# Kernel optimization log

Measured on AMD Instinct MI355X. Metric: run time of the kernel, lower is better.

Reference implementation:

```python
import jax, jax.numpy as jnp
import numpy as np

D_MODEL = 256
NHEAD = 4
K_MODE = 8


def setup_inputs() -> dict:
    key = jax.random.key(0)
    ks = jax.random.split(key, 12)
    bs, S = 2, 4096
    inp = {
        "q": jax.random.normal(ks[0], (bs, S, D_MODEL), jnp.float32),
        "k": jax.random.normal(ks[1], (bs, S, D_MODEL + K_MODE), jnp.float32),
        "v": jax.random.normal(ks[2], (bs, S, D_MODEL), jnp.float32),
        "mask": jax.random.randint(ks[3], (bs, S, S), 0, 2, jnp.int32),
        # nn.Linear params: W is [out, in], y = x @ W.T + b
        "Wq": jax.random.normal(ks[4], (D_MODEL, D_MODEL), jnp.float32) * 0.02,
        "bq": jnp.zeros((D_MODEL,), jnp.float32),
        "Wk": jax.random.normal(ks[5], (D_MODEL, D_MODEL + K_MODE), jnp.float32) * 0.02,
        "bk": jnp.zeros((D_MODEL,), jnp.float32),
        "Wv": jax.random.normal(ks[6], (D_MODEL, D_MODEL), jnp.float32) * 0.02,
        "bv": jnp.zeros((D_MODEL,), jnp.float32),
        "Wo": jax.random.normal(ks[7], (D_MODEL, NHEAD * D_MODEL), jnp.float32) * 0.02,
        "bo": jnp.zeros((D_MODEL,), jnp.float32),
    }
    return inp


def reference(q, k, v, mask, Wq, bq, Wk, bk, Wv, bv, Wo, bo):
    # Projections (nn.Linear: x @ W.T + b). In the original module the projected
    # q/k/v are repeat-broadcast identically across all nhead heads (d_k = d_model),
    # and the mask broadcasts across heads too (dropout disabled). Hence every head
    # computes the exact same attention output; we compute it once and tile the
    # concat, which is mathematically identical and avoids redundant HBM traffic.
    qh = jnp.einsum('bsd,ed->bse', q, Wq) + bq   # [bs, S, d]
    kh = jnp.einsum('bsd,ed->bse', k, Wk) + bk   # [bs, S, d]
    vh = jnp.einsum('bsd,ed->bse', v, Wv) + bv   # [bs, S, d]

    scale = 1.0 / jnp.sqrt(jnp.asarray(D_MODEL, qh.dtype))
    scores = jnp.einsum('bqd,bkd->bqk', qh, kh) * scale  # [bs, S, S]
    scores = jnp.where(mask == 0, jnp.asarray(-1e9, scores.dtype), scores)
    attn = jax.nn.softmax(scores, axis=-1)
    per_head = jnp.einsum('bqk,bkd->bqd', attn, vh)      # [bs, S, d]

    concat = jnp.tile(per_head, (1, 1, NHEAD))           # [bs, S, h*d]
    return jnp.einsum('bsf,df->bsd', concat, Wo) + bo
```

## Files before the change

### kernel.cpp

```cpp
#include <hip/hip_runtime.h>

typedef unsigned short u16;
typedef unsigned int u32;
typedef unsigned long long u64;
typedef __bf16 bf16x8 __attribute__((ext_vector_type(8)));
typedef float f32x4 __attribute__((ext_vector_type(4)));

#define S_LEN 4096
#define DM 256

__device__ __forceinline__ u16 f2b(float f) {
  u32 u = __builtin_bit_cast(u32, f);
  u = (u + 0x7FFFu + ((u >> 16) & 1u)) >> 16;
  return (u16)u;
}
__device__ __forceinline__ float b2f(u16 b) {
  return __builtin_bit_cast(float, (u32)b << 16);
}

__device__ __forceinline__ f32x4 mfma16(bf16x8 a, bf16x8 b, f32x4 c) {
  return __builtin_amdgcn_mfma_f32_16x16x32_bf16(a, b, c, 0, 0, 0);
}

__device__ __forceinline__ void gl_lds16(const u16* g, u16* l) {
  __builtin_amdgcn_global_load_lds(
      (const __attribute__((address_space(1))) u32*)g,
      (__attribute__((address_space(3))) u32*)l, 16, 0, 0);
}

#define SB() __builtin_amdgcn_sched_barrier(0)

template <int TIN_F32, int TOUT_F32, int BIAS_MODE>
__global__ __launch_bounds__(256, 2) void gemm_nt_kernel(
    const void* __restrict__ Ap, const void* __restrict__ Bp,
    void* __restrict__ Cp, const float* __restrict__ bias, float scale,
    int M, int N, int K, int lda, int ldb, int ldc,
    long sA, long sB, long sC) {
  __shared__ u16 As[64][72];
  __shared__ u16 Bs[64][72];
  const int tid = threadIdx.x;
  const int w = tid >> 6, ln = tid & 63, lg = ln >> 4, ll = ln & 15;
  const int m0 = blockIdx.x * 64, n0 = blockIdx.y * 64;
  const long zA = (long)blockIdx.z * sA, zB = (long)blockIdx.z * sB,
             zC = (long)blockIdx.z * sC;

  const f32x4 fzero = {0.f, 0.f, 0.f, 0.f};
  f32x4 acc[4];
#pragma unroll
  for (int i = 0; i < 4; ++i) acc[i] = fzero;

  const int srow = tid >> 2, scb = (tid & 3) * 16;
  const int nk = (K + 63) >> 6;
  for (int kc = 0; kc < nk; ++kc) {
    const int k0 = kc * 64;
    if (TIN_F32) {
      {
        const float* src = (const float*)Ap + zA + (size_t)(m0 + srow) * lda + k0 + scb;
        u16 t[16];
        if (k0 + 64 <= K) {
#pragma unroll
          for (int i = 0; i < 16; ++i) t[i] = f2b(src[i]);
        } else {
#pragma unroll
          for (int i = 0; i < 16; ++i) {
            int gk = k0 + scb + i;
            t[i] = (gk < K) ? f2b(src[i]) : (u16)0;
          }
        }
#pragma unroll
        for (int i = 0; i < 16; ++i) As[srow][scb + i] = t[i];
      }
      {
        const float* src = (const float*)Bp + zB + (size_t)(n0 + srow) * ldb + k0 + scb;
        u16 t[16];
        if (k0 + 64 <= K) {
#pragma unroll
          for (int i = 0; i < 16; ++i) t[i] = f2b(src[i]);
        } else {
#pragma unroll
          for (int i = 0; i < 16; ++i) {
            int gk = k0 + scb + i;
            t[i] = (gk < K) ? f2b(src[i]) : (u16)0;
          }
        }
#pragma unroll
        for (int i = 0; i < 16; ++i) Bs[srow][scb + i] = t[i];
      }
    } else {
      const u16* srcA = (const u16*)Ap + zA + (size_t)(m0 + srow) * lda + k0 + scb;
      *(bf16x8*)&As[srow][scb] = *(const bf16x8*)srcA;
      *(bf16x8*)&As[srow][scb + 8] = *(const bf16x8*)(srcA + 8);
      const u16* srcB = (const u16*)Bp + zB + (size_t)(n0 + srow) * ldb + k0 + scb;
      *(bf16x8*)&Bs[srow][scb] = *(const bf16x8*)srcB;
      *(bf16x8*)&Bs[srow][scb + 8] = *(const bf16x8*)(srcB + 8);
    }
    __syncthreads();
#pragma unroll
    for (int ks = 0; ks < 2; ++ks) {
      bf16x8 af = *(const bf16x8*)&As[w * 16 + ll][ks * 32 + lg * 8];
#pragma unroll
      for (int ct = 0; ct < 4; ++ct) {
        bf16x8 bfr = *(const bf16x8*)&Bs[ct * 16 + ll][ks * 32 + lg * 8];
        acc[ct] = mfma16(af, bfr, acc[ct]);
      }
    }
    __syncthreads();
  }

#pragma unroll
  for (int ct = 0; ct < 4; ++ct) {
#pragma unroll
    for (int j = 0; j < 4; ++j) {
      int row = m0 + w * 16 + lg * 4 + j;
      int col = n0 + ct * 16 + ll;
      float v = acc[ct][j];
      if (BIAS_MODE == 1) v += bias[col];
      if (BIAS_MODE == 2) v += bias[row];
      v *= scale;
      if (TOUT_F32)
        ((float*)Cp)[zC + (size_t)row * ldc + col] = v;
      else
        ((u16*)Cp)[zC + (size_t)row * ldc + col] = f2b(v);
    }
  }
}

__global__ void wos_kernel(const float* __restrict__ Wo, u16* __restrict__ WoS) {
  int d = blockIdx.x, e = threadIdx.x;
  const float* p = Wo + (size_t)d * 1024;
  WoS[(size_t)d * 256 + e] = f2b(p[e] + p[256 + e] + p[512 + e] + p[768 + e]);
}

__global__ __launch_bounds__(256) void bitpack_kernel(const int* __restrict__ mask,
                                                      u32* __restrict__ mb) {
  const int ln = threadIdx.x & 63;
  const int gw = (int)((blockIdx.x * 256 + threadIdx.x) >> 6);
  const int nw = gridDim.x * 4;
  u64* mb64 = (u64*)mb;
  for (int it = gw; it < 131072; it += nw) {
    const int* p = mask + (size_t)it * 256 + ln;
    int v0 = p[0], v1 = p[64], v2 = p[128], v3 = p[192];
    u64 b0 = __ballot(v0 != 0);
    u64 b1 = __ballot(v1 != 0);
    u64 b2 = __ballot(v2 != 0);
    u64 b3 = __ballot(v3 != 0);
    if (ln < 4) {
      u64 val = ln == 0 ? b0 : (ln == 1 ? b1 : (ln == 2 ? b2 : b3));
      mb64[(size_t)it * 4 + ln] = val;
    }
  }
}

__global__ __launch_bounds__(256, 2) void flash_kernel(
    const u16* __restrict__ qh, const u16* __restrict__ kh,
    const u16* __restrict__ vhT, const u32* __restrict__ mb,
    u16* __restrict__ Opart, float* __restrict__ Lpart) {
  __shared__ u16 kh_s[2][32 * 256];
  __shared__ u16 vs_s[2][256 * 32];
  __shared__ u16 p_s[4][32][40];

  const int tid = threadIdx.x;
  const int w = tid >> 6, ln = tid & 63, lg = ln >> 4, ll = ln & 15;
  const int wg = ((int)blockIdx.x & 7) * 64 + ((int)blockIdx.x >> 3);
  const int q0 = (wg & 31) * 128;
  const int b = (wg >> 5) & 1;
  const int h = wg >> 6;

  bf16x8 qf[2][8];
#pragma unroll
  for (int qg = 0; qg < 2; ++qg) {
    const u16* qp = qh + (size_t)(b * S_LEN + q0 + w * 32 + qg * 16 + ll) * DM + lg * 8;
#pragma unroll
    for (int ks = 0; ks < 8; ++ks) qf[qg][ks] = *(const bf16x8*)(qp + ks * 32);
  }

  const f32x4 fzero = {0.f, 0.f, 0.f, 0.f};
  f32x4 acc_o[2][16];
#pragma unroll
  for (int qg = 0; qg < 2; ++qg)
#pragma unroll
    for (int i = 0; i < 16; ++i) acc_o[qg][i] = fzero;
  float l_run[2][4] = {{0.f, 0.f, 0.f, 0.f}, {0.f, 0.f, 0.f, 0.f}};

  const u16* kbase = kh + (size_t)(b * S_LEN + h * 512) * DM;
  const u16* vbase = vhT + (size_t)b * DM * S_LEN + h * 512;
  const u32* mbase = mb + (size_t)(b * S_LEN + q0 + w * 32) * 128 + h * 16;

  auto stage = [&](int t, int buf) {
#pragma unroll
    for (int i = 0; i < 4; ++i) {
      int c = i * 256 + tid;
      int row = c >> 5, ccl = c & 31;
      int ccg = ccl ^ (row & 7);
      gl_lds16(kbase + (size_t)(t * 32 + row) * DM + ccg * 8,
               &kh_s[buf][(i * 256 + w * 64) * 8]);
    }
#pragma unroll
    for (int i = 0; i < 4; ++i) {
      int c = i * 256 + tid;
      int row = c >> 2, ccl = c & 3;
      int ccg = ccl ^ ((row >> 1) & 3);
      gl_lds16(vbase + (size_t)row * S_LEN + t * 32 + ccg * 8,
               &vs_s[buf][(i * 256 + w * 64) * 8]);
    }
  };

  u32 mwc[2][4], mwn[2][4];
  auto loadmask = [&](int t, u32 out[2][4]) {
#pragma unroll
    for (int qg = 0; qg < 2; ++qg)
#pragma unroll
      for (int j = 0; j < 4; ++j)
        out[qg][j] = mbase[(size_t)(qg * 16 + lg * 4 + j) * 128 + t];
  };

  stage(0, 0);
  asm volatile("s_waitcnt vmcnt(0)" ::: "memory");
  __builtin_amdgcn_s_barrier();
  SB();
  loadmask(0, mwc);
  SB();
  stage(1, 1);
  SB();

  int cur = 0;

#define QK_PHASE()                                                            \
  f32x4 accs[2][2];                                                           \
  accs[0][0] = fzero; accs[0][1] = fzero;                                     \
  accs[1][0] = fzero; accs[1][1] = fzero;                                     \
  __builtin_amdgcn_s_setprio(1);                                              \
  _Pragma("unroll") for (int ks = 0; ks < 8; ++ks) {                          \
    _Pragma("unroll") for (int half = 0; half < 2; ++half) {                  \
      int krow = half * 16 + ll;                                              \
      bf16x8 kf = *(const bf16x8*)&kh_s[cur][krow * 256 +                     \
                                            (((ks * 4 + lg) ^ (krow & 7)) << 3)]; \
      accs[0][half] = mfma16(qf[0][ks], kf, accs[0][half]);                   \
      accs[1][half] = mfma16(qf[1][ks], kf, accs[1][half]);                   \
    }                                                                         \
  }                                                                           \
  __builtin_amdgcn_s_setprio(0);

#define SM_PV_PHASE()                                                         \
  _Pragma("unroll") for (int qg = 0; qg < 2; ++qg) {                          \
    _Pragma("unroll") for (int j = 0; j < 4; ++j) {                           \
      u32 m = mwc[qg][j];                                                     \
      float p0 = ((m >> ll) & 1u) ? __expf(accs[qg][0][j]) : 0.f;             \
      float p1 = ((m >> (16 + ll)) & 1u) ? __expf(accs[qg][1][j]) : 0.f;      \
      l_run[qg][j] += p0 + p1;                                                \
      int r = qg * 16 + lg * 4 + j;                                           \
      p_s[w][r][ll] = f2b(p0);                                                \
      p_s[w][r][16 + ll] = f2b(p1);                                           \
    }                                                                         \
  }                                                                           \
  bf16x8 pf0 = *(const bf16x8*)&p_s[w][ll][lg * 8];                           \
  bf16x8 pf1 = *(const bf16x8*)&p_s[w][16 + ll][lg * 8];                      \
  __builtin_amdgcn_s_setprio(1);                                              \
  _Pragma("unroll") for (int dt = 0; dt < 16; ++dt) {                         \
    int vrow = dt * 16 + ll;                                                  \
    bf16x8 vf = *(const bf16x8*)&vs_s[cur][vrow * 32 +                        \
                                          ((lg ^ ((vrow >> 1) & 3)) << 3)];   \
    acc_o[0][dt] = mfma16(pf0, vf, acc_o[0][dt]);                             \
    acc_o[1][dt] = mfma16(pf1, vf, acc_o[1][dt]);                             \
  }                                                                           \
  __builtin_amdgcn_s_setprio(0);

#define COPY_MW()                                                             \
  _Pragma("unroll") for (int qg = 0; qg < 2; ++qg)                            \
  _Pragma("unroll") for (int j = 0; j < 4; ++j) mwc[qg][j] = mwn[qg][j];

#pragma unroll 1
  for (int t = 0; t < 14; ++t) {
    {
      QK_PHASE();
      asm volatile("s_waitcnt vmcnt(8)" ::: "memory");
      SB();
      SM_PV_PHASE();
    }
    SB();
    __builtin_amdgcn_s_barrier();
    SB();
    loadmask(t + 1, mwn);
    SB();
    stage(t + 2, cur);
    SB();
    asm volatile("s_waitcnt vmcnt(16)" ::: "memory");
    SB();
    __builtin_amdgcn_s_barrier();
    SB();
    COPY_MW();
    cur ^= 1;
  }

  {
    {
      QK_PHASE();
      asm volatile("s_waitcnt vmcnt(8)" ::: "memory");
      SB();
      SM_PV_PHASE();
    }
    SB();
    __builtin_amdgcn_s_barrier();
    SB();
    loadmask(15, mwn);
    SB();
    asm volatile("s_waitcnt vmcnt(8)" ::: "memory");
    SB();
    __builtin_amdgcn_s_barrier();
    SB();
    COPY_MW();
    cur ^= 1;
  }

  {
    QK_PHASE();
    asm volatile("s_waitcnt vmcnt(0)" ::: "memory");
    SB();
    SM_PV_PHASE();
  }

#pragma unroll
  for (int qg = 0; qg < 2; ++qg) {
#pragma unroll
    for (int j = 0; j < 4; ++j) {
      float l = l_run[qg][j];
      l += __shfl_xor(l, 1);
      l += __shfl_xor(l, 2);
      l += __shfl_xor(l, 4);
      l += __shfl_xor(l, 8);
      l_run[qg][j] = l;
    }
  }
  const size_t growb = (size_t)h * 8192 + (size_t)b * S_LEN + q0 + w * 32;
  if (ll == 0) {
#pragma unroll
    for (int qg = 0; qg < 2; ++qg)
#pragma unroll
      for (int j = 0; j < 4; ++j)
        Lpart[growb + qg * 16 + lg * 4 + j] = l_run[qg][j];
  }
#pragma unroll
  for (int qg = 0; qg < 2; ++qg)
#pragma unroll
    for (int dt = 0; dt < 16; ++dt)
#pragma unroll
      for (int j = 0; j < 4; ++j)
        Opart[(growb + qg * 16 + lg * 4 + j) * 256 + dt * 16 + ll] =
            f2b(acc_o[qg][dt][j]);
}

__global__ void combine_kernel(const u16* __restrict__ Opart,
                               const float* __restrict__ Lpart,
                               u16* __restrict__ ph) {
  const int r = blockIdx.x;
  const int d = threadIdx.x;
  float o = 0.f, l = 0.f;
#pragma unroll
  for (int s = 0; s < 8; ++s) {
    l += Lpart[(size_t)s * 8192 + r];
    o += b2f(Opart[((size_t)s * 8192 + r) * 256 + d]);
  }
  ph[(size_t)r * 256 + d] = f2b(o / l);
}

extern "C" void kernel_launch(void* const* d_in, const int* in_sizes, int n_in,
                              void* d_out, int out_size, void* d_ws, size_t ws_size,
                              hipStream_t stream) {
  const float* q = (const float*)d_in[0];
  const float* k = (const float*)d_in[1];
  const float* v = (const float*)d_in[2];
  const int* mask = (const int*)d_in[3];
  const float* Wq = (const float*)d_in[4];
  const float* bq = (const float*)d_in[5];
  const float* Wk = (const float*)d_in[6];
  const float* bk = (const float*)d_in[7];
  const float* Wv = (const float*)d_in[8];
  const float* bv = (const float*)d_in[9];
  const float* Wo = (const float*)d_in[10];
  const float* bo = (const float*)d_in[11];

  char* ws = (char*)d_ws;
  u16* qh = (u16*)(ws + 0);
  u16* kh = (u16*)(ws + 4194304);
  u16* vhT = (u16*)(ws + 8388608);
  u16* WoS = (u16*)(ws + 12582912);
  u32* mb = (u32*)(ws + 12713984);
  u16* Op = (u16*)(ws + 16908288);
  float* Lp = (float*)(ws + 50462720);

  dim3 blk(256);
  gemm_nt_kernel<1, 0, 1><<<dim3(128, 4, 1), blk, 0, stream>>>(
      q, Wq, qh, bq, 0.0625f, 8192, 256, 256, 256, 256, 256, 0, 0, 0);
  gemm_nt_kernel<1, 0, 1><<<dim3(128, 4, 1), blk, 0, stream>>>(
      k, Wk, kh, bk, 1.0f, 8192, 256, 264, 264, 264, 256, 0, 0, 0);
  gemm_nt_kernel<1, 0, 2><<<dim3(4, 64, 2), blk, 0, stream>>>(
      Wv, v, vhT, bv, 1.0f, 256, 4096, 256, 256, 256, 4096,
      0, (long)4096 * 256, (long)256 * 4096);
  wos_kernel<<<dim3(256), blk, 0, stream>>>(Wo, WoS);
  bitpack_kernel<<<dim3(2048), blk, 0, stream>>>(mask, mb);
  flash_kernel<<<dim3(512), blk, 0, stream>>>(qh, kh, vhT, mb, Op, Lp);
  combine_kernel<<<dim3(8192), blk, 0, stream>>>(Op, Lp, qh);
  gemm_nt_kernel<0, 1, 1><<<dim3(128, 4, 1), blk, 0, stream>>>(
      qh, WoS, d_out, bo, 1.0f, 8192, 256, 256, 256, 256, 256, 0, 0, 0);
}
```

Baseline: 137.2 us.

## Single-buffer K/V LDS with split staging, raise occupancy and KV split count

Drops the double-buffered K/V shared-memory tiles in favour of single buffers. K and V loads are now issued separately, so the next K tile streams in during the softmax/PV phase and the next V tile during the following QK phase. Launch bounds go from 2 to 3 blocks per CU. When the workspace is large enough, the KV sequence is split 16 ways instead of 8, doubling the grid to 1024 blocks, and the combine kernel sums a runtime number of partial slots. This trades overlap depth and more partial-output traffic for higher occupancy and more parallel blocks.

```diff
diff --git a/kernel.cpp b/kernel.cpp
--- a/kernel.cpp
+++ b/kernel.cpp
@@ -151,17 +151,19 @@
   }
 }
 
-__global__ __launch_bounds__(256, 2) void flash_kernel(
+__global__ __launch_bounds__(256, 3) void flash_kernel(
     const u16* __restrict__ qh, const u16* __restrict__ kh,
     const u16* __restrict__ vhT, const u32* __restrict__ mb,
-    u16* __restrict__ Opart, float* __restrict__ Lpart) {
-  __shared__ u16 kh_s[2][32 * 256];
-  __shared__ u16 vs_s[2][256 * 32];
+    u16* __restrict__ Opart, float* __restrict__ Lpart,
+    int ckv, int ntiles) {
+  __shared__ u16 kh_s[32 * 256];
+  __shared__ u16 vs_s[256 * 32];
   __shared__ u16 p_s[4][32][40];
 
   const int tid = threadIdx.x;
   const int w = tid >> 6, ln = tid & 63, lg = ln >> 4, ll = ln & 15;
-  const int wg = ((int)blockIdx.x & 7) * 64 + ((int)blockIdx.x >> 3);
+  const int nwg = gridDim.x;
+  const int wg = ((int)blockIdx.x & 7) * (nwg >> 3) + ((int)blockIdx.x >> 3);
   const int q0 = (wg & 31) * 128;
   const int b = (wg >> 5) & 1;
   const int h = wg >> 6;
@@ -182,59 +184,46 @@
     for (int i = 0; i < 16; ++i) acc_o[qg][i] = fzero;
   float l_run[2][4] = {{0.f, 0.f, 0.f, 0.f}, {0.f, 0.f, 0.f, 0.f}};
 
-  const u16* kbase = kh + (size_t)(b * S_LEN + h * 512) * DM;
-  const u16* vbase = vhT + (size_t)b * DM * S_LEN + h * 512;
-  const u32* mbase = mb + (size_t)(b * S_LEN + q0 + w * 32) * 128 + h * 16;
-
-  auto stage = [&](int t, int buf) {
+  const u16* kbase = kh + (size_t)(b * S_LEN + h * ckv) * DM;
+  const u16* vbase = vhT + (size_t)b * DM * S_LEN + h * ckv;
+  const u32* mbase = mb + (size_t)(b * S_LEN + q0 + w * 32) * 128 + (h * ckv >> 5);
+
+  auto stageK = [&](int t) {
 #pragma unroll
     for (int i = 0; i < 4; ++i) {
       int c = i * 256 + tid;
       int row = c >> 5, ccl = c & 31;
       int ccg = ccl ^ (row & 7);
       gl_lds16(kbase + (size_t)(t * 32 + row) * DM + ccg * 8,
-               &kh_s[buf][(i * 256 + w * 64) * 8]);
-    }
+               &kh_s[(i * 256 + w * 64) * 8]);
+    }
+  };
+  auto stageV = [&](int t) {
 #pragma unroll
     for (int i = 0; i < 4; ++i) {
       int c = i * 256 + tid;
       int row = c >> 2, ccl = c & 3;
       int ccg = ccl ^ ((row >> 1) & 3);
       gl_lds16(vbase + (size_t)row * S_LEN + t * 32 + ccg * 8,
-               &vs_s[buf][(i * 256 + w * 64) * 8]);
+               &vs_s[(i * 256 + w * 64) * 8]);
     }
   };
 
-  u32 mwc[2][4], mwn[2][4];
-  auto loadmask = [&](int t, u32 out[2][4]) {
-#pragma unroll
-    for (int qg = 0; qg < 2; ++qg)
-#pragma unroll
-      for (int j = 0; j < 4; ++j)
-        out[qg][j] = mbase[(size_t)(qg * 16 + lg * 4 + j) * 128 + t];
-  };
-
-  stage(0, 0);
-  asm volatile("s_waitcnt vmcnt(0)" ::: "memory");
-  __builtin_amdgcn_s_barrier();
-  SB();
-  loadmask(0, mwc);
-  SB();
-  stage(1, 1);
-  SB();
-
-  int cur = 0;
+  u32 mwc[2][4];
+#define LOADMASK(t)                                                           \
+  _Pragma("unroll") for (int qg = 0; qg < 2; ++qg)                            \
+  _Pragma("unroll") for (int j = 0; j < 4; ++j)                               \
+      mwc[qg][j] = mbase[(size_t)(qg * 16 + lg * 4 + j) * 128 + (t)];
 
 #define QK_PHASE()                                                            \
-  f32x4 accs[2][2];                                                           \
   accs[0][0] = fzero; accs[0][1] = fzero;                                     \
   accs[1][0] = fzero; accs[1][1] = fzero;                                     \
   __builtin_amdgcn_s_setprio(1);                                              \
   _Pragma("unroll") for (int ks = 0; ks < 8; ++ks) {                          \
     _Pragma("unroll") for (int half = 0; half < 2; ++half) {                  \
       int krow = half * 16 + ll;                                              \
-      bf16x8 kf = *(const bf16x8*)&kh_s[cur][krow * 256 +                     \
-                                            (((ks * 4 + lg) ^ (krow & 7)) << 3)]; \
+      bf16x8 kf = *(const bf16x8*)&kh_s[krow * 256 +                          \
+                                        (((ks * 4 + lg) ^ (krow & 7)) << 3)]; \
       accs[0][half] = mfma16(qf[0][ks], kf, accs[0][half]);                   \
       accs[1][half] = mfma16(qf[1][ks], kf, accs[1][half]);                   \
     }                                                                         \
@@ -258,62 +247,53 @@
   __builtin_amdgcn_s_setprio(1);                                              \
   _Pragma("unroll") for (int dt = 0; dt < 16; ++dt) {                         \
     int vrow = dt * 16 + ll;                                                  \
-    bf16x8 vf = *(const bf16x8*)&vs_s[cur][vrow * 32 +                        \
-                                          ((lg ^ ((vrow >> 1) & 3)) << 3)];   \
+    bf16x8 vf = *(const bf16x8*)&vs_s[vrow * 32 +                             \
+                                      ((lg ^ ((vrow >> 1) & 3)) << 3)];       \
     acc_o[0][dt] = mfma16(pf0, vf, acc_o[0][dt]);                             \
     acc_o[1][dt] = mfma16(pf1, vf, acc_o[1][dt]);                             \
   }                                                                           \
   __builtin_amdgcn_s_setprio(0);
 
-#define COPY_MW()                                                             \
-  _Pragma("unroll") for (int qg = 0; qg < 2; ++qg)                            \
-  _Pragma("unroll") for (int j = 0; j < 4; ++j) mwc[qg][j] = mwn[qg][j];
+  stageK(0);
+  SB();
+  stageV(0);
+  SB();
+  LOADMASK(0);
+  SB();
 
 #pragma unroll 1
-  for (int t = 0; t < 14; ++t) {
-    {
-      QK_PHASE();
-      asm volatile("s_waitcnt vmcnt(8)" ::: "memory");
-      SB();
-      SM_PV_PHASE();
-    }
+  for (int t = 0; t < ntiles - 1; ++t) {
+    asm volatile("s_waitcnt vmcnt(12)" ::: "memory");
     SB();
     __builtin_amdgcn_s_barrier();
     SB();
-    loadmask(t + 1, mwn);
-    SB();
-    stage(t + 2, cur);
-    SB();
-    asm volatile("s_waitcnt vmcnt(16)" ::: "memory");
+    f32x4 accs[2][2];
+    QK_PHASE();
     SB();
     __builtin_amdgcn_s_barrier();
     SB();
-    COPY_MW();
-    cur ^= 1;
+    stageK(t + 1);
+    SB();
+    asm volatile("s_waitcnt vmcnt(4)" ::: "memory");
+    SB();
+    SM_PV_PHASE();
+    SB();
+    __builtin_amdgcn_s_barrier();
+    SB();
+    LOADMASK(t + 1);
+    SB();
+    stageV(t + 1);
+    SB();
   }
 
   {
-    {
-      QK_PHASE();
-      asm volatile("s_waitcnt vmcnt(8)" ::: "memory");
-      SB();
-      SM_PV_PHASE();
-    }
+    asm volatile("s_waitcnt vmcnt(12)" ::: "memory");
     SB();
     __builtin_amdgcn_s_barrier();
     SB();
-    loadmask(15, mwn);
-    SB();
-    asm volatile("s_waitcnt vmcnt(8)" ::: "memory");
-    SB();
-    __builtin_amdgcn_s_barrier();
-    SB();
-    COPY_MW();
-    cur ^= 1;
-  }
-
-  {
+    f32x4 accs[2][2];
     QK_PHASE();
+    SB();
     asm volatile("s_waitcnt vmcnt(0)" ::: "memory");
     SB();
     SM_PV_PHASE();
@@ -351,12 +331,11 @@
 
 __global__ void combine_kernel(const u16* __restrict__ Opart,
                                const float* __restrict__ Lpart,
-                               u16* __restrict__ ph) {
+                               u16* __restrict__ ph, int nslots) {
   const int r = blockIdx.x;
   const int d = threadIdx.x;
   float o = 0.f, l = 0.f;
-#pragma unroll
-  for (int s = 0; s < 8; ++s) {
+  for (int s = 0; s < nslots; ++s) {
     l += Lpart[(size_t)s * 8192 + r];
     o += b2f(Opart[((size_t)s * 8192 + r) * 256 + d]);
   }
@@ -386,7 +365,9 @@
   u16* WoS = (u16*)(ws + 12582912);
   u32* mb = (u32*)(ws + 12713984);
   u16* Op = (u16*)(ws + 16908288);
-  float* Lp = (float*)(ws + 50462720);
+  int nslots = (ws_size >= 84541440u) ? 16 : 8;
+  float* Lp = (float*)(ws + 16908288 + (size_t)nslots * 8192 * 256 * 2);
+  int ckv = S_LEN / nslots, ntiles = ckv / 32;
 
   dim3 blk(256);
   gemm_nt_kernel<1, 0, 1><<<dim3(128, 4, 1), blk, 0, stream>>>(
@@ -398,8 +379,9 @@
       0, (long)4096 * 256, (long)256 * 4096);
   wos_kernel<<<dim3(256), blk, 0, stream>>>(Wo, WoS);
   bitpack_kernel<<<dim3(2048), blk, 0, stream>>>(mask, mb);
-  flash_kernel<<<dim3(512), blk, 0, stream>>>(qh, kh, vhT, mb, Op, Lp);
-  combine_kernel<<<dim3(8192), blk, 0, stream>>>(Op, Lp, qh);
+  flash_kernel<<<dim3(64 * nslots), blk, 0, stream>>>(qh, kh, vhT, mb, Op, Lp,
+                                                      ckv, ntiles);
+  combine_kernel<<<dim3(8192), blk, 0, stream>>>(Op, Lp, qh, nslots);
   gemm_nt_kernel<0, 1, 1><<<dim3(128, 4, 1), blk, 0, stream>>>(
       qh, WoS, d_out, bo, 1.0f, 8192, 256, 256, 256, 256, 256, 0, 0, 0);
 }
```

Result: slower. 381.9 us (+178.3%).
